# Kernel tuning notes

Hardware: AMD Instinct MI355X
Metric: run time of the kernel (lower is better)

## Reference

```python
import jax, jax.numpy as jnp
import numpy as np

H = 32  # LSTM_HIDDEN


def setup_inputs() -> dict:
    key = jax.random.key(0)
    ks = jax.random.split(key, 8)
    B, T = 2048, 1024
    x = jax.random.normal(ks[0], (B, T, H), dtype=jnp.float32)
    # prefix mask from random lengths in [1, T] (pack_padded_sequence semantics)
    lengths = jax.random.randint(ks[1], (B,), 1, T + 1)
    mask = (jnp.arange(T)[None, :] < lengths[:, None]).astype(jnp.float32)
    s = float(1.0 / np.sqrt(H))  # torch LSTM/Linear default init scale
    u = lambda k, shape: jax.random.uniform(k, shape, jnp.float32, -s, s)
    return {
        'sequence_batch': x,
        'sequence_mask': mask,
        'w_ih': u(ks[2], (4 * H, H)),
        'w_hh': u(ks[3], (4 * H, H)),
        'b_ih': u(ks[4], (4 * H,)),
        'b_hh': u(ks[5], (4 * H,)),
        'w_cls': u(ks[6], (1, H)),
        'b_cls': u(ks[7], (1,)),
    }


def _lstm_masked(x, mask, w_ih, w_hh, b_ih, b_hh):
    """Single-layer LSTM over padded batch; outputs zeroed at padded steps.

    Equivalent to pack_padded_sequence -> nn.LSTM -> pad_packed_sequence for
    the returned per-step outputs (padded positions are zero; pooled mean
    ignores them). PyTorch gate order: i, f, g, o.
    """
    B, T, _ = x.shape
    # precompute input contribution for all steps: [B, T, 4H]
    xg = jnp.einsum('bti,gi->btg', x, w_ih) + (b_ih + b_hh)

    def step(carry, xg_t):
        h, c = carry
        g = xg_t + h @ w_hh.T  # [B, 4H]
        i, f, gc, o = jnp.split(g, 4, axis=-1)
        c = jax.nn.sigmoid(f) * c + jax.nn.sigmoid(i) * jnp.tanh(gc)
        h = jax.nn.sigmoid(o) * jnp.tanh(c)
        return (h, c), h

    h0 = jnp.zeros((B, H), x.dtype)
    _, hs = jax.lax.scan(step, (h0, h0), jnp.swapaxes(xg, 0, 1))  # [T, B, H]
    hs = jnp.swapaxes(hs, 0, 1)  # [B, T, H]
    return hs * mask[..., None]


def reference(sequence_batch, sequence_mask, w_ih, w_hh, b_ih, b_hh, w_cls, b_cls):
    outs = _lstm_masked(sequence_batch, sequence_mask, w_ih, w_hh, b_ih, b_hh)
    # masked mean pool (outs already zeroed at padded positions)
    denom = jnp.clip(sequence_mask.sum(axis=1, keepdims=True), 1e-8, None)
    pooled = outs.sum(axis=1) / denom  # [B, H]
    probs = jax.nn.sigmoid(pooled @ w_cls.T + b_cls)  # [B, 1]
    return pooled, probs
```

## Files before the change

kernel.cpp:

```cpp
#include <hip/hip_runtime.h>


__device__ __forceinline__ float fast_sigmoid(float x) {
    return __builtin_amdgcn_rcpf(1.0f + __expf(-x));
}
__device__ __forceinline__ float fast_tanh(float x) {
    return fmaf(2.0f, fast_sigmoid(2.0f * x), -1.0f);
}
__device__ __forceinline__ float lane_bcast(float v, int srclane) {
    return __int_as_float(__builtin_amdgcn_readlane(__float_as_int(v), srclane));
}

#define R16A(M) M(0) M(1) M(2) M(3) M(4) M(5) M(6) M(7) \
                M(8) M(9) M(10) M(11) M(12) M(13) M(14) M(15)
#define R16B(M) M(16) M(17) M(18) M(19) M(20) M(21) M(22) M(23) \
                M(24) M(25) M(26) M(27) M(28) M(29) M(30) M(31)
#define R32(M) R16A(M) R16B(M)

#define DECLW(i) float wiA_##i, whA_##i, wiB_##i, whB_##i;
#define LOADW(i) wiA_##i = w_ih[rA32 + (i)]; whA_##i = w_hh[rA32 + (i)]; \
                 wiB_##i = w_ih[rB32 + (i)]; whB_##i = w_hh[rB32 + (i)];

#define XP0(i) { const float xm = lane_bcast(xq, i); \
                 axA0n = fmaf(xm, wiA_##i, axA0n); axB0n = fmaf(xm, wiB_##i, axB0n); }
#define XP1(i) { const float xm = lane_bcast(xq, i); \
                 axA1n = fmaf(xm, wiA_##i, axA1n); axB1n = fmaf(xm, wiB_##i, axB1n); }
#define HP0(i) { const float hm = lane_bcast(h, i); \
                 ahA0 = fmaf(hm, whA_##i, ahA0); ahB0 = fmaf(hm, whB_##i, ahB0); }
#define HP1(i) { const float hm = lane_bcast(h, i); \
                 ahA1 = fmaf(hm, whA_##i, ahA1); ahB1 = fmaf(hm, whB_##i, ahB1); }

__global__ __launch_bounds__(64)
void len_kernel(const float* __restrict__ mask, int* __restrict__ lens, int B, int T)
{
    const int b = blockIdx.x;
    if (b >= B) return;
    const int lane = threadIdx.x;
    const float4* m4 = (const float4*)(mask + (size_t)b * T);
    float s = 0.0f;
    for (int i = lane; i < (T >> 2); i += 64) {
        const float4 v = m4[i];
        s += (v.x + v.y) + (v.z + v.w);
    }
#pragma unroll
    for (int off = 32; off > 0; off >>= 1) s += __shfl_down(s, off, 64);
    if (lane == 0) lens[b] = (int)(s + 0.5f);
}

__global__ __launch_bounds__(1024)
void sort_kernel(const int* __restrict__ lens, int* __restrict__ sortedIdx, int B, int T)
{
    __shared__ int hist[1024];
    __shared__ int scan[1024];
    __shared__ int cur[1024];
    const int tid = threadIdx.x;
    if (tid < T) hist[tid] = 0;
    __syncthreads();
    for (int b = tid; b < B; b += blockDim.x)
        atomicAdd(&hist[lens[b] - 1], 1);
    __syncthreads();
    if (tid < T) scan[tid] = hist[tid];
    __syncthreads();
    for (int off = 1; off < T; off <<= 1) {
        int v = 0;
        if (tid >= off && tid < T) v = scan[tid - off];
        __syncthreads();
        if (tid < T) scan[tid] += v;
        __syncthreads();
    }
    if (tid < T) cur[tid] = scan[tid] - hist[tid];
    __syncthreads();
    for (int b = tid; b < B; b += blockDim.x) {
        const int pos = atomicAdd(&cur[lens[b] - 1], 1);
        sortedIdx[pos] = b;
    }
}

__global__ __launch_bounds__(64, 2)
void lstm_main(const float* __restrict__ x,
               const int* __restrict__ lens,
               const int* __restrict__ sortedIdx,
               const float* __restrict__ w_ih,
               const float* __restrict__ w_hh,
               const float* __restrict__ b_ih,
               const float* __restrict__ b_hh,
               const float* __restrict__ w_cls,
               const float* __restrict__ b_cls,
               float* __restrict__ out,
               int B, int T)
{
    const int p = blockIdx.x;
    const int lane = threadIdx.x;
    const int lm = lane & 31;
    const int rA32 = lane * 32;
    const int rB32 = (lane + 64) * 32;
    const int Tm1 = T - 1;

    R32(DECLW)
    R32(LOADW)
    const float bA = b_ih[lane] + b_hh[lane];
    const float bB = b_ih[lane + 64] + b_hh[lane + 64];

    for (int s = 0; s < 2; ++s) {
        const int b = sortedIdx[s == 0 ? p : (B - 1 - p)];
        const int L = lens[b];
        const float* xb = x + (size_t)b * T * 32;

        float h = 0.0f, c = 0.0f, hsum = 0.0f;

        float xq = xb[lm];
        float axA0n = bA, axA1n = 0.f, axB0n = bB, axB1n = 0.f;
        R16A(XP0) R16B(XP1)
        float axA0c = axA0n, axA1c = axA1n, axB0c = axB0n, axB1c = axB1n;
        xq = xb[min(1, Tm1) * 32 + lm];

        for (int t = 0; t < L; ++t) {
            const float xn = xb[min(t + 2, Tm1) * 32 + lm];
            float ahA0 = 0.f, ahA1 = 0.f, ahB0 = 0.f, ahB1 = 0.f;
            R16A(HP0) R16B(HP1)
            const float accA = (axA0c + ahA0) + (axA1c + ahA1);
            const float accB = (axB0c + ahB0) + (axB1c + ahB1);
            const float accA2 = __shfl_xor(accA, 32, 64);
            const float accB2 = __shfl_xor(accB, 32, 64);
            const float ig = fast_sigmoid(accA);
            const float fg = fast_sigmoid(accA2);
            const float gg = fast_tanh(accB);
            const float og = fast_sigmoid(accB2);
            c = fg * c + ig * gg;
            h = og * fast_tanh(c);
            hsum += h;
            axA0n = bA; axA1n = 0.f; axB0n = bB; axB1n = 0.f;
            R16A(XP0) R16B(XP1)
            axA0c = axA0n; axA1c = axA1n; axB0c = axB0n; axB1c = axB1n;
            xq = xn;
        }

        const float Lf = (float)L;
        const float pooled = hsum / Lf;
        if (lane < 32) out[(size_t)b * 32 + lane] = pooled;

        float contrib = (lane < 32) ? pooled * w_cls[lane] : 0.0f;
#pragma unroll
        for (int off = 32; off > 0; off >>= 1)
            contrib += __shfl_down(contrib, off, 64);
        if (lane == 0)
            out[(size_t)B * 32 + b] = fast_sigmoid(contrib + b_cls[0]);
    }
}

extern "C" void kernel_launch(void* const* d_in, const int* in_sizes, int n_in,
                              void* d_out, int out_size, void* d_ws, size_t ws_size,
                              hipStream_t stream)
{
    const float* x     = (const float*)d_in[0];
    const float* mask  = (const float*)d_in[1];
    const float* w_ih  = (const float*)d_in[2];
    const float* w_hh  = (const float*)d_in[3];
    const float* b_ih  = (const float*)d_in[4];
    const float* b_hh  = (const float*)d_in[5];
    const float* w_cls = (const float*)d_in[6];
    const float* b_cls = (const float*)d_in[7];
    float* out = (float*)d_out;

    const int B = out_size / 33;
    const int T = in_sizes[1] / B;

    int* lens = (int*)d_ws;
    int* sidx = lens + B;

    len_kernel<<<B, 64, 0, stream>>>(mask, lens, B, T);
    sort_kernel<<<1, 1024, 0, stream>>>(lens, sidx, B, T);
    lstm_main<<<B / 2, 64, 0, stream>>>(x, lens, sidx, w_ih, w_hh, b_ih, b_hh,
                                        w_cls, b_cls, out, B, T);
}
```

Measured before the change: 922.6 us.

## Interleave two LSTM sequences per wave with atomic work queue scheduling

Each wave now advances two independent sequences step by step, interleaved, so that their serial recurrences can hide each other's latency. Work is handed out through an atomic counter in longest-first order instead of fixed long/short pairs per block. The counter is reset inside len_kernel. The input and hidden projections are fused into one broadcast loop with four accumulators per gate half, and weight registers are pinned with empty asm. Launch bounds drop to one wave per SIMD, which raises register pressure and depends on the atomic counter being reset correctly.

Result: slower. 1.012 ms (+9.7%).

```diff
diff --git a/kernel.cpp b/kernel.cpp
--- a/kernel.cpp
+++ b/kernel.cpp
@@ -20,20 +20,71 @@
 #define DECLW(i) float wiA_##i, whA_##i, wiB_##i, whB_##i;
 #define LOADW(i) wiA_##i = w_ih[rA32 + (i)]; whA_##i = w_hh[rA32 + (i)]; \
                  wiB_##i = w_ih[rB32 + (i)]; whB_##i = w_hh[rB32 + (i)];
-
-#define XP0(i) { const float xm = lane_bcast(xq, i); \
-                 axA0n = fmaf(xm, wiA_##i, axA0n); axB0n = fmaf(xm, wiB_##i, axB0n); }
-#define XP1(i) { const float xm = lane_bcast(xq, i); \
-                 axA1n = fmaf(xm, wiA_##i, axA1n); axB1n = fmaf(xm, wiB_##i, axB1n); }
-#define HP0(i) { const float hm = lane_bcast(h, i); \
-                 ahA0 = fmaf(hm, whA_##i, ahA0); ahB0 = fmaf(hm, whB_##i, ahB0); }
-#define HP1(i) { const float hm = lane_bcast(h, i); \
-                 ahA1 = fmaf(hm, whA_##i, ahA1); ahB1 = fmaf(hm, whB_##i, ahB1); }
+#define PINW(i)  asm volatile("" : "+v"(wiA_##i)); asm volatile("" : "+v"(whA_##i)); \
+                 asm volatile("" : "+v"(wiB_##i)); asm volatile("" : "+v"(whB_##i));
+
+#define FXH0(i) { const float xm = lane_bcast(xcur, i); const float hm = lane_bcast(hcur, i); \
+    aA0 = fmaf(xm, wiA_##i, aA0); aA1 = fmaf(hm, whA_##i, aA1); \
+    aB0 = fmaf(xm, wiB_##i, aB0); aB1 = fmaf(hm, whB_##i, aB1); }
+#define FXH1(i) { const float xm = lane_bcast(xcur, i); const float hm = lane_bcast(hcur, i); \
+    aA2 = fmaf(xm, wiA_##i, aA2); aA3 = fmaf(hm, whA_##i, aA3); \
+    aB2 = fmaf(xm, wiB_##i, aB2); aB3 = fmaf(hm, whB_##i, aB3); }
+
+#define STEP(s) { \
+    const float xn_ = xb##s[min(t##s + 2, Tm1) * 32 + lm]; \
+    const float hcur = h##s, xcur = xq##s; \
+    float aA0 = bA, aA1 = 0.f, aA2 = 0.f, aA3 = 0.f; \
+    float aB0 = bB, aB1 = 0.f, aB2 = 0.f, aB3 = 0.f; \
+    R16A(FXH0) R16B(FXH1) \
+    const float accA  = (aA0 + aA1) + (aA2 + aA3); \
+    const float accB  = (aB0 + aB1) + (aB2 + aB3); \
+    const float accA2 = __shfl_xor(accA, 32, 64); \
+    const float accB2 = __shfl_xor(accB, 32, 64); \
+    const float ig = fast_sigmoid(accA); \
+    const float fg = fast_sigmoid(accA2); \
+    const float gg = fast_tanh(accB); \
+    const float og = fast_sigmoid(accB2); \
+    c##s = fg * c##s + ig * gg; \
+    h##s = og * fast_tanh(c##s); \
+    hsum##s += h##s; \
+    xq##s = xp##s; xp##s = xn_; \
+    ++t##s; \
+}
+
+#define FINISH(s) { \
+    const float pooled = hsum##s / (float)L##s; \
+    if (lane < 32) out[(size_t)b##s * 32 + lane] = pooled; \
+    float contrib = (lane < 32) ? pooled * wcls : 0.0f; \
+    contrib += __shfl_down(contrib, 32, 64); \
+    contrib += __shfl_down(contrib, 16, 64); \
+    contrib += __shfl_down(contrib, 8, 64); \
+    contrib += __shfl_down(contrib, 4, 64); \
+    contrib += __shfl_down(contrib, 2, 64); \
+    contrib += __shfl_down(contrib, 1, 64); \
+    if (lane == 0) out[(size_t)B * 32 + b##s] = fast_sigmoid(contrib + bcls); \
+}
+
+#define PRIME(s) if (b##s >= 0) { \
+    L##s = lens[b##s]; t##s = 0; \
+    xb##s = x + (size_t)b##s * T * 32; \
+    h##s = 0.f; c##s = 0.f; hsum##s = 0.f; \
+    xq##s = xb##s[lm]; \
+    xp##s = xb##s[min(1, Tm1) * 32 + lm]; \
+}
+
+#define POP(s) { \
+    int p_ = 0; \
+    if (lane == 0) p_ = atomicAdd(counter, 1); \
+    p_ = __shfl(p_, 0, 64); \
+    b##s = (p_ < B) ? sidx[B - 1 - p_] : -1; \
+}
 
 __global__ __launch_bounds__(64)
-void len_kernel(const float* __restrict__ mask, int* __restrict__ lens, int B, int T)
+void len_kernel(const float* __restrict__ mask, int* __restrict__ lens,
+                int* __restrict__ counter, int B, int T)
 {
     const int b = blockIdx.x;
+    if (b == 0 && threadIdx.x == 0) *counter = 0;
     if (b >= B) return;
     const int lane = threadIdx.x;
     const float4* m4 = (const float4*)(mask + (size_t)b * T);
@@ -76,10 +127,11 @@
     }
 }
 
-__global__ __launch_bounds__(64, 2)
+__global__ __launch_bounds__(64, 1)
 void lstm_main(const float* __restrict__ x,
                const int* __restrict__ lens,
-               const int* __restrict__ sortedIdx,
+               const int* __restrict__ sidx,
+               int* __restrict__ counter,
                const float* __restrict__ w_ih,
                const float* __restrict__ w_hh,
                const float* __restrict__ b_ih,
@@ -89,7 +141,6 @@
                float* __restrict__ out,
                int B, int T)
 {
-    const int p = blockIdx.x;
     const int lane = threadIdx.x;
     const int lm = lane & 31;
     const int rA32 = lane * 32;
@@ -98,53 +149,36 @@
 
     R32(DECLW)
     R32(LOADW)
+    R32(PINW)
     const float bA = b_ih[lane] + b_hh[lane];
     const float bB = b_ih[lane + 64] + b_hh[lane + 64];
-
-    for (int s = 0; s < 2; ++s) {
-        const int b = sortedIdx[s == 0 ? p : (B - 1 - p)];
-        const int L = lens[b];
-        const float* xb = x + (size_t)b * T * 32;
-
-        float h = 0.0f, c = 0.0f, hsum = 0.0f;
-
-        float xq = xb[lm];
-        float axA0n = bA, axA1n = 0.f, axB0n = bB, axB1n = 0.f;
-        R16A(XP0) R16B(XP1)
-        float axA0c = axA0n, axA1c = axA1n, axB0c = axB0n, axB1c = axB1n;
-        xq = xb[min(1, Tm1) * 32 + lm];
-
-        for (int t = 0; t < L; ++t) {
-            const float xn = xb[min(t + 2, Tm1) * 32 + lm];
-            float ahA0 = 0.f, ahA1 = 0.f, ahB0 = 0.f, ahB1 = 0.f;
-            R16A(HP0) R16B(HP1)
-            const float accA = (axA0c + ahA0) + (axA1c + ahA1);
-            const float accB = (axB0c + ahB0) + (axB1c + ahB1);
-            const float accA2 = __shfl_xor(accA, 32, 64);
-            const float accB2 = __shfl_xor(accB, 32, 64);
-            const float ig = fast_sigmoid(accA);
-            const float fg = fast_sigmoid(accA2);
-            const float gg = fast_tanh(accB);
-            const float og = fast_sigmoid(accB2);
-            c = fg * c + ig * gg;
-            h = og * fast_tanh(c);
-            hsum += h;
-            axA0n = bA; axA1n = 0.f; axB0n = bB; axB1n = 0.f;
-            R16A(XP0) R16B(XP1)
-            axA0c = axA0n; axA1c = axA1n; axB0c = axB0n; axB1c = axB1n;
-            xq = xn;
-        }
-
-        const float Lf = (float)L;
-        const float pooled = hsum / Lf;
-        if (lane < 32) out[(size_t)b * 32 + lane] = pooled;
-
-        float contrib = (lane < 32) ? pooled * w_cls[lane] : 0.0f;
-#pragma unroll
-        for (int off = 32; off > 0; off >>= 1)
-            contrib += __shfl_down(contrib, off, 64);
-        if (lane == 0)
-            out[(size_t)B * 32 + b] = fast_sigmoid(contrib + b_cls[0]);
+    const float wcls = w_cls[lm];
+    const float bcls = b_cls[0];
+
+    int b0, b1;
+    int L0 = 0, t0 = 0, L1 = 0, t1 = 0;
+    const float *xb0 = x, *xb1 = x;
+    float h0 = 0.f, c0 = 0.f, hsum0 = 0.f, xq0 = 0.f, xp0 = 0.f;
+    float h1 = 0.f, c1 = 0.f, hsum1 = 0.f, xq1 = 0.f, xp1 = 0.f;
+
+    POP(0) POP(1)
+    PRIME(0) PRIME(1)
+
+    while (b0 >= 0 && b1 >= 0) {
+        const int K = min(L0 - t0, L1 - t1);
+        for (int k = 0; k < K; ++k) { STEP(0) STEP(1) }
+        if (t0 >= L0) { FINISH(0) POP(0) PRIME(0) }
+        if (t1 >= L1) { FINISH(1) POP(1) PRIME(1) }
+    }
+    while (b0 >= 0) {
+        const int K = L0 - t0;
+        for (int k = 0; k < K; ++k) { STEP(0) }
+        FINISH(0) POP(0) PRIME(0)
+    }
+    while (b1 >= 0) {
+        const int K = L1 - t1;
+        for (int k = 0; k < K; ++k) { STEP(1) }
+        FINISH(1) POP(1) PRIME(1)
     }
 }
 
@@ -165,11 +199,12 @@
     const int B = out_size / 33;
     const int T = in_sizes[1] / B;
 
-    int* lens = (int*)d_ws;
-    int* sidx = lens + B;
-
-    len_kernel<<<B, 64, 0, stream>>>(mask, lens, B, T);
+    int* lens    = (int*)d_ws;
+    int* sidx    = lens + B;
+    int* counter = sidx + B;
+
+    len_kernel<<<B, 64, 0, stream>>>(mask, lens, counter, B, T);
     sort_kernel<<<1, 1024, 0, stream>>>(lens, sidx, B, T);
-    lstm_main<<<B / 2, 64, 0, stream>>>(x, lens, sidx, w_ih, w_hh, b_ih, b_hh,
-                                        w_cls, b_cls, out, B, T);
-}
+    lstm_main<<<2048, 64, 0, stream>>>(x, lens, sidx, counter, w_ih, w_hh,
+                                       b_ih, b_hh, w_cls, b_cls, out, B, T);
+}
```

## Interleave input and recurrent FMAs in one loop; deepen x prefetch; pin weights

Applied to the files above, without the earlier changes.

The input projection used to be computed off the critical path, after the gates, for the next step. Now it is folded into the same unrolled loop as the recurrent matvec, with four independent accumulators per gate half. The x prefetch distance grows from two steps to four, weight registers are pinned with empty asm constraints, and waves_per_eu is forced to 1. This aims at more instruction-level parallelism per step at the cost of occupancy. It also puts the x FMAs back on the serial dependency chain of each timestep, which could lengthen it.

Result: slower. 974.2 us (+5.6%).

```diff
diff --git a/kernel.cpp b/kernel.cpp
--- a/kernel.cpp
+++ b/kernel.cpp
@@ -20,15 +20,15 @@
 #define DECLW(i) float wiA_##i, whA_##i, wiB_##i, whB_##i;
 #define LOADW(i) wiA_##i = w_ih[rA32 + (i)]; whA_##i = w_hh[rA32 + (i)]; \
                  wiB_##i = w_ih[rB32 + (i)]; whB_##i = w_hh[rB32 + (i)];
+#define PINW(i)  asm volatile("" : "+v"(wiA_##i)); asm volatile("" : "+v"(whA_##i)); \
+                 asm volatile("" : "+v"(wiB_##i)); asm volatile("" : "+v"(whB_##i));
 
-#define XP0(i) { const float xm = lane_bcast(xq, i); \
-                 axA0n = fmaf(xm, wiA_##i, axA0n); axB0n = fmaf(xm, wiB_##i, axB0n); }
-#define XP1(i) { const float xm = lane_bcast(xq, i); \
-                 axA1n = fmaf(xm, wiA_##i, axA1n); axB1n = fmaf(xm, wiB_##i, axB1n); }
-#define HP0(i) { const float hm = lane_bcast(h, i); \
-                 ahA0 = fmaf(hm, whA_##i, ahA0); ahB0 = fmaf(hm, whB_##i, ahB0); }
-#define HP1(i) { const float hm = lane_bcast(h, i); \
-                 ahA1 = fmaf(hm, whA_##i, ahA1); ahB1 = fmaf(hm, whB_##i, ahB1); }
+#define FXH0(i) { const float xm = lane_bcast(xcur, i); const float hm = lane_bcast(hcur, i); \
+    aA0 = fmaf(xm, wiA_##i, aA0); aA1 = fmaf(hm, whA_##i, aA1); \
+    aB0 = fmaf(xm, wiB_##i, aB0); aB1 = fmaf(hm, whB_##i, aB1); }
+#define FXH1(i) { const float xm = lane_bcast(xcur, i); const float hm = lane_bcast(hcur, i); \
+    aA2 = fmaf(xm, wiA_##i, aA2); aA3 = fmaf(hm, whA_##i, aA3); \
+    aB2 = fmaf(xm, wiB_##i, aB2); aB3 = fmaf(hm, whB_##i, aB3); }
 
 __global__ __launch_bounds__(64)
 void len_kernel(const float* __restrict__ mask, int* __restrict__ lens, int B, int T)
@@ -76,10 +76,11 @@
     }
 }
 
-__global__ __launch_bounds__(64, 2)
+__global__ __launch_bounds__(64)
+__attribute__((amdgpu_waves_per_eu(1, 1)))
 void lstm_main(const float* __restrict__ x,
                const int* __restrict__ lens,
-               const int* __restrict__ sortedIdx,
+               const int* __restrict__ sidx,
                const float* __restrict__ w_ih,
                const float* __restrict__ w_hh,
                const float* __restrict__ b_ih,
@@ -98,28 +99,31 @@
 
     R32(DECLW)
     R32(LOADW)
+    R32(PINW)
     const float bA = b_ih[lane] + b_hh[lane];
     const float bB = b_ih[lane + 64] + b_hh[lane + 64];
+    const float wcls = w_cls[lm];
+    const float bcls = b_cls[0];
 
     for (int s = 0; s < 2; ++s) {
-        const int b = sortedIdx[s == 0 ? p : (B - 1 - p)];
+        const int b = sidx[s == 0 ? p : (B - 1 - p)];
         const int L = lens[b];
         const float* xb = x + (size_t)b * T * 32;
 
         float h = 0.0f, c = 0.0f, hsum = 0.0f;
-
         float xq = xb[lm];
-        float axA0n = bA, axA1n = 0.f, axB0n = bB, axB1n = 0.f;
-        R16A(XP0) R16B(XP1)
-        float axA0c = axA0n, axA1c = axA1n, axB0c = axB0n, axB1c = axB1n;
-        xq = xb[min(1, Tm1) * 32 + lm];
+        float xo = xb[32 + lm];
+        float xp = xb[min(2, Tm1) * 32 + lm];
+        float xp2 = xb[min(3, Tm1) * 32 + lm];
 
         for (int t = 0; t < L; ++t) {
-            const float xn = xb[min(t + 2, Tm1) * 32 + lm];
-            float ahA0 = 0.f, ahA1 = 0.f, ahB0 = 0.f, ahB1 = 0.f;
-            R16A(HP0) R16B(HP1)
-            const float accA = (axA0c + ahA0) + (axA1c + ahA1);
-            const float accB = (axB0c + ahB0) + (axB1c + ahB1);
+            const float xn_ = xb[min(t + 4, Tm1) * 32 + lm];
+            const float hcur = h, xcur = xq;
+            float aA0 = bA, aA1 = 0.f, aA2 = 0.f, aA3 = 0.f;
+            float aB0 = bB, aB1 = 0.f, aB2 = 0.f, aB3 = 0.f;
+            R16A(FXH0) R16B(FXH1)
+            const float accA  = (aA0 + aA1) + (aA2 + aA3);
+            const float accB  = (aB0 + aB1) + (aB2 + aB3);
             const float accA2 = __shfl_xor(accA, 32, 64);
             const float accB2 = __shfl_xor(accB, 32, 64);
             const float ig = fast_sigmoid(accA);
@@ -129,22 +133,18 @@
             c = fg * c + ig * gg;
             h = og * fast_tanh(c);
             hsum += h;
-            axA0n = bA; axA1n = 0.f; axB0n = bB; axB1n = 0.f;
-            R16A(XP0) R16B(XP1)
-            axA0c = axA0n; axA1c = axA1n; axB0c = axB0n; axB1c = axB1n;
-            xq = xn;
+            xq = xo; xo = xp; xp = xp2; xp2 = xn_;
         }
 
-        const float Lf = (float)L;
-        const float pooled = hsum / Lf;
+        const float pooled = hsum / (float)L;
         if (lane < 32) out[(size_t)b * 32 + lane] = pooled;
 
-        float contrib = (lane < 32) ? pooled * w_cls[lane] : 0.0f;
+        float contrib = (lane < 32) ? pooled * wcls : 0.0f;
 #pragma unroll
         for (int off = 32; off > 0; off >>= 1)
             contrib += __shfl_down(contrib, off, 64);
         if (lane == 0)
-            out[(size_t)B * 32 + b] = fast_sigmoid(contrib + b_cls[0]);
+            out[(size_t)B * 32 + b] = fast_sigmoid(contrib + bcls);
     }
 }
 
```
